# Kernel tuning notes

Hardware: AMD Instinct MI355X
Metric: run time of the kernel (lower is better)

Reference implementation:

```python
import jax, jax.numpy as jnp
import numpy as np

N = 50000
E = 600000
D = 128


def setup_inputs() -> dict:
    key = jax.random.key(0)
    ks = jax.random.split(key, 10)
    scale = 1.0 / np.sqrt(D)
    inp = {
        "x": jax.random.normal(ks[0], (N, D), dtype=jnp.float32),
        "edge_index": jax.random.randint(ks[1], (2, E), 0, N, dtype=jnp.int64),
        # layer 0: fc + res_fc (residual=True, activation=relu)
        "W1": jax.random.normal(ks[2], (D, D), dtype=jnp.float32) * scale,
        "R1": jax.random.normal(ks[3], (D, D), dtype=jnp.float32) * scale,
        # layer 1
        "W2": jax.random.normal(ks[4], (D, D), dtype=jnp.float32) * scale,
        "R2": jax.random.normal(ks[5], (D, D), dtype=jnp.float32) * scale,
        # layer 2 (last, encoding=False -> no residual/activation)
        "W3": jax.random.normal(ks[6], (D, D), dtype=jnp.float32) * scale,
        # head Linear(out_dim, out_dim) with bias
        "Wh": jax.random.normal(ks[7], (D, D), dtype=jnp.float32) * scale,
        "bh": jnp.zeros((D,), dtype=jnp.float32),
    }
    return inp


def _gcn_stack(x, row, col, norm, W1, R1, W2, R2, W3, Wh, bh):
    n = x.shape[0]

    def conv(x, W, R, act):
        h = x @ W                                   # [N, D]
        msg = h[row] * norm[:, None]                # gather + per-edge scale [E+N, D]
        agg = jax.ops.segment_sum(msg, col, num_segments=n)  # scatter-add [N, D]
        if R is not None:
            agg = agg + x @ R                       # residual
        if act:
            agg = jax.nn.relu(agg)
        return agg

    x = conv(x, W1, R1, True)
    x = conv(x, W2, R2, True)
    x = conv(x, W3, None, False)
    return x @ Wh + bh


def reference(x, edge_index, W1, R1, W2, R2, W3, Wh, bh):
    n = x.shape[0]
    # add self loops (same edge structure for every layer)
    loops = jnp.arange(n, dtype=edge_index.dtype)
    row = jnp.concatenate([edge_index[0], loops])
    col = jnp.concatenate([edge_index[1], loops])
    # symmetric degree normalization: deg computed over col (incl. self loops)
    deg = jax.ops.segment_sum(jnp.ones_like(col, dtype=x.dtype), col, num_segments=n)
    dinv = deg ** -0.5
    norm = dinv[row] * dinv[col]                    # [E+N]
    return _gcn_stack(x, row, col, norm, W1, R1, W2, R2, W3, Wh, bh)
```

## Files before the change

### kernel.cpp

```cpp
#include <hip/hip_runtime.h>
#include <hip/hip_bf16.h>


#define SCAN_CHUNK 1024

typedef _Float16 half8 __attribute__((ext_vector_type(8)));
typedef _Float16 half4 __attribute__((ext_vector_type(4)));
typedef float floatx4 __attribute__((ext_vector_type(4)));

__global__ __launch_bounds__(256) void prep0_kernel(
        int* __restrict__ cnt, int n, int nzb,
        const float* __restrict__ W1, const float* __restrict__ R1,
        const float* __restrict__ W2, const float* __restrict__ R2,
        const float* __restrict__ W3, const float* __restrict__ Wh,
        _Float16* __restrict__ Wt) {
    int b = blockIdx.x;
    int t = threadIdx.x;
    if (b < nzb) {
        int i = b * 256 + t;
        if (i < n) cnt[i] = 0;
        return;
    }
    int b2 = b - nzb;
    if (b2 < 64) {
        __shared__ float tile[32][33];
        int mat = b2 >> 4, tl = b2 & 15;
        const float* W = (mat == 0) ? W1 : (mat == 1) ? R1 : (mat == 2) ? W2 : R2;
        _Float16* T = Wt + (size_t)mat * 16384;
        int tr = (tl >> 2) * 32, tc = (tl & 3) * 32;
        int i = t >> 3, j4 = t & 7;
        float4 v = *(const float4*)&W[(tr + i) * 128 + tc + j4 * 4];
        tile[i][j4 * 4 + 0] = v.x;
        tile[i][j4 * 4 + 1] = v.y;
        tile[i][j4 * 4 + 2] = v.z;
        tile[i][j4 * 4 + 3] = v.w;
        __syncthreads();
        half4 h;
        h.x = (_Float16)tile[j4 * 4 + 0][i];
        h.y = (_Float16)tile[j4 * 4 + 1][i];
        h.z = (_Float16)tile[j4 * 4 + 2][i];
        h.w = (_Float16)tile[j4 * 4 + 3][i];
        *(half4*)&T[(tc + i) * 128 + tr + j4 * 4] = h;
    } else {
        int bb = b2 - 64;
        _Float16* Wtc = Wt + (size_t)4 * 16384;
        int c = bb * 8 + (t >> 5);
        int k0 = (t & 31) * 4;
        float acc0 = 0.f, acc1 = 0.f, acc2 = 0.f, acc3 = 0.f;
        for (int j = 0; j < 128; ++j) {
            float wh = Wh[j * 128 + c];
            acc0 = fmaf(W3[(k0 + 0) * 128 + j], wh, acc0);
            acc1 = fmaf(W3[(k0 + 1) * 128 + j], wh, acc1);
            acc2 = fmaf(W3[(k0 + 2) * 128 + j], wh, acc2);
            acc3 = fmaf(W3[(k0 + 3) * 128 + j], wh, acc3);
        }
        half4 h;
        h.x = (_Float16)acc0; h.y = (_Float16)acc1;
        h.z = (_Float16)acc2; h.w = (_Float16)acc3;
        *(half4*)&Wtc[c * 128 + k0] = h;
    }
}

__global__ void hist_kernel(const int* __restrict__ col, int* __restrict__ cnt, int E) {
    int i = blockIdx.x * blockDim.x + threadIdx.x;
    if (i < E) atomicAdd(&cnt[col[i]], 1);
}

__global__ __launch_bounds__(256) void scan_fused_kernel(
        const int* __restrict__ cnt, int* __restrict__ row_ptr,
        int* __restrict__ cursor, float* __restrict__ dinv, int n, int E) {
    __shared__ int s[256];
    int b = blockIdx.x, t = threadIdx.x;

    int tot = 0;
    int lim = b * SCAN_CHUNK;
    for (int i = t * 4; i < lim; i += 1024) {
        int4 q = *(const int4*)&cnt[i];
        tot += q.x + q.y + q.z + q.w;
    }
    s[t] = tot;
    __syncthreads();
    for (int off = 128; off > 0; off >>= 1) {
        if (t < off) s[t] += s[t + off];
        __syncthreads();
    }
    int boffb = s[0];
    __syncthreads();

    int base = b * SCAN_CHUNK + t * 4;
    int v[4];
    int sum = 0;
    for (int i = 0; i < 4; ++i) {
        v[i] = (base + i < n) ? cnt[base + i] : 0;
        sum += v[i];
    }
    s[t] = sum;
    __syncthreads();
    for (int off = 1; off < 256; off <<= 1) {
        int add = (t >= off) ? s[t - off] : 0;
        __syncthreads();
        s[t] += add;
        __syncthreads();
    }
    int prefix = boffb + ((t == 0) ? 0 : s[t - 1]);
    for (int i = 0; i < 4; ++i) {
        if (base + i < n) {
            row_ptr[base + i] = prefix;
            cursor[base + i] = prefix;
            dinv[base + i] = rsqrtf((float)(v[i] + 1));
            prefix += v[i];
        }
    }
    if (b == 0 && t == 0) row_ptr[n] = E;
}

__global__ void fill_kernel(const int* __restrict__ row, const int* __restrict__ colv,
                            int* __restrict__ cursor,
                            unsigned short* __restrict__ csr, int E) {
    int i = blockIdx.x * blockDim.x + threadIdx.x;
    if (i < E) {
        int c = colv[i];
        int p = atomicAdd(&cursor[c], 1);
        csr[p] = (unsigned short)row[i];
    }
}

template <int F32IN>
__global__ __launch_bounds__(256) void gemm_dual_kernel(
        const void* __restrict__ Xv, const _Float16* __restrict__ WtA,
        const _Float16* __restrict__ WtB, _Float16* __restrict__ outA,
        _Float16* __restrict__ outB, const float* __restrict__ dinv, int n) {
    __shared__ _Float16 Af[64 * 136];
    __shared__ _Float16 Bt[128 * 136];
    int t = threadIdx.x;
    int r0 = blockIdx.x * 64;

    if (F32IN) {
        const float* X = (const float*)Xv;
#pragma unroll
        for (int i = 0; i < 8; ++i) {
            int flat = i * 256 + t;
            int r = flat >> 5, c4 = flat & 31;
            float4 v = make_float4(0.f, 0.f, 0.f, 0.f);
            if (r0 + r < n) v = ((const float4*)X)[(size_t)(r0 + r) * 32 + c4];
            half4 h;
            h.x = (_Float16)v.x; h.y = (_Float16)v.y;
            h.z = (_Float16)v.z; h.w = (_Float16)v.w;
            *(half4*)&Af[r * 136 + c4 * 4] = h;
        }
    } else {
        const _Float16* X = (const _Float16*)Xv;
#pragma unroll
        for (int i = 0; i < 4; ++i) {
            int flat = i * 256 + t;
            int r = flat >> 4, k8 = flat & 15;
            half8 v = {0, 0, 0, 0, 0, 0, 0, 0};
            if (r0 + r < n) v = *(const half8*)&X[(size_t)(r0 + r) * 128 + k8 * 8];
            *(half8*)&Af[r * 136 + k8 * 8] = v;
        }
    }
#pragma unroll
    for (int i = 0; i < 8; ++i) {
        int flat = i * 256 + t;
        int c = flat >> 4, k8 = flat & 15;
        *(half8*)&Bt[c * 136 + k8 * 8] = *(const half8*)&WtA[c * 128 + k8 * 8];
    }
    __syncthreads();

    int lane = t & 63, w = t >> 6;
    int m = lane & 15, q = lane >> 4;
    int rowb = r0 + w * 16 + q * 4;

    float dv[4];
#pragma unroll
    for (int r = 0; r < 4; ++r) {
        int gr = rowb + r;
        dv[r] = (gr < n) ? dinv[gr] : 0.f;
    }

    half8 a[4];
#pragma unroll
    for (int s = 0; s < 4; ++s)
        a[s] = *(const half8*)&Af[(w * 16 + m) * 136 + s * 32 + q * 8];

    floatx4 acc[8];
#pragma unroll
    for (int nt = 0; nt < 8; ++nt) acc[nt] = (floatx4){0.f, 0.f, 0.f, 0.f};
#pragma unroll
    for (int s = 0; s < 4; ++s)
#pragma unroll
        for (int nt = 0; nt < 8; ++nt) {
            half8 b = *(const half8*)&Bt[(nt * 16 + m) * 136 + s * 32 + q * 8];
            acc[nt] = __builtin_amdgcn_mfma_f32_16x16x32_f16(a[s], b, acc[nt], 0, 0, 0);
        }
    __syncthreads();
#pragma unroll
    for (int i = 0; i < 8; ++i) {
        int flat = i * 256 + t;
        int c = flat >> 4, k8 = flat & 15;
        *(half8*)&Bt[c * 136 + k8 * 8] = *(const half8*)&WtB[c * 128 + k8 * 8];
    }
#pragma unroll
    for (int nt = 0; nt < 8; ++nt) {
        int col = nt * 16 + m;
#pragma unroll
        for (int r = 0; r < 4; ++r) {
            int gr = rowb + r;
            if (gr < n) outA[(size_t)gr * 128 + col] = (_Float16)(acc[nt][r] * dv[r]);
        }
    }
    __syncthreads();

#pragma unroll
    for (int nt = 0; nt < 8; ++nt) acc[nt] = (floatx4){0.f, 0.f, 0.f, 0.f};
#pragma unroll
    for (int s = 0; s < 4; ++s)
#pragma unroll
        for (int nt = 0; nt < 8; ++nt) {
            half8 b = *(const half8*)&Bt[(nt * 16 + m) * 136 + s * 32 + q * 8];
            acc[nt] = __builtin_amdgcn_mfma_f32_16x16x32_f16(a[s], b, acc[nt], 0, 0, 0);
        }
#pragma unroll
    for (int nt = 0; nt < 8; ++nt) {
        int col = nt * 16 + m;
#pragma unroll
        for (int r = 0; r < 4; ++r) {
            int gr = rowb + r;
            if (gr < n) outB[(size_t)gr * 128 + col] = (_Float16)acc[nt][r];
        }
    }
}

__global__ __launch_bounds__(256) void gemm_h_kernel(
        const _Float16* __restrict__ X, const _Float16* __restrict__ Wt,
        _Float16* __restrict__ out, const float* __restrict__ dinv, int n) {
    __shared__ _Float16 Af[64 * 136];
    __shared__ _Float16 Bt[128 * 136];
    int t = threadIdx.x;
    int r0 = blockIdx.x * 64;

#pragma unroll
    for (int i = 0; i < 4; ++i) {
        int flat = i * 256 + t;
        int r = flat >> 4, k8 = flat & 15;
        half8 v = {0, 0, 0, 0, 0, 0, 0, 0};
        if (r0 + r < n) v = *(const half8*)&X[(size_t)(r0 + r) * 128 + k8 * 8];
        *(half8*)&Af[r * 136 + k8 * 8] = v;
    }
#pragma unroll
    for (int i = 0; i < 8; ++i) {
        int flat = i * 256 + t;
        int c = flat >> 4, k8 = flat & 15;
        *(half8*)&Bt[c * 136 + k8 * 8] = *(const half8*)&Wt[c * 128 + k8 * 8];
    }
    __syncthreads();

    int lane = t & 63, w = t >> 6;
    int m = lane & 15, q = lane >> 4;
    int rowb = r0 + w * 16 + q * 4;

    float dv[4];
#pragma unroll
    for (int r = 0; r < 4; ++r) {
        int gr = rowb + r;
        dv[r] = (gr < n) ? dinv[gr] : 0.f;
    }

    floatx4 acc[8];
#pragma unroll
    for (int nt = 0; nt < 8; ++nt) acc[nt] = (floatx4){0.f, 0.f, 0.f, 0.f};

#pragma unroll
    for (int s = 0; s < 4; ++s) {
        half8 a = *(const half8*)&Af[(w * 16 + m) * 136 + s * 32 + q * 8];
#pragma unroll
        for (int nt = 0; nt < 8; ++nt) {
            half8 b = *(const half8*)&Bt[(nt * 16 + m) * 136 + s * 32 + q * 8];
            acc[nt] = __builtin_amdgcn_mfma_f32_16x16x32_f16(a, b, acc[nt], 0, 0, 0);
        }
    }

#pragma unroll
    for (int nt = 0; nt < 8; ++nt) {
        int col = nt * 16 + m;
#pragma unroll
        for (int r = 0; r < 4; ++r) {
            int gr = rowb + r;
            if (gr < n) out[(size_t)gr * 128 + col] = (_Float16)(acc[nt][r] * dv[r]);
        }
    }
}

template <int RELU, int FINAL>
__global__ void spmm_kernel(const _Float16* __restrict__ h, const _Float16* __restrict__ xr,
                            const int* __restrict__ row_ptr,
                            const unsigned short* __restrict__ csr,
                            const float* __restrict__ dinv, _Float16* __restrict__ outh,
                            float* __restrict__ outf, const float* __restrict__ bias,
                            int n) {
    int gid = blockIdx.x * blockDim.x + threadIdx.x;
    int node = gid >> 4;
    int fl = gid & 15;
    if (node >= n) return;
    const half8* hp8 = (const half8*)h;

    float acc[8];
#pragma unroll
    for (int j = 0; j < 8; ++j) acc[j] = 0.f;

    int e0 = row_ptr[node], e1 = row_ptr[node + 1];
    for (int e = e0; e < e1; e += 8) {
        int src[8];
        float nn[8];
#pragma unroll
        for (int u = 0; u < 8; ++u) {
            int idx = e + u;
            int act = idx < e1;
            src[u] = csr[act ? idx : e];
            nn[u] = act ? 1.f : 0.f;
        }
        half8 v[8];
#pragma unroll
        for (int u = 0; u < 8; ++u)
            v[u] = hp8[(size_t)src[u] * 16 + fl];
#pragma unroll
        for (int u = 0; u < 8; ++u)
#pragma unroll
            for (int j = 0; j < 8; ++j)
                acc[j] = fmaf(nn[u], (float)v[u][j], acc[j]);
    }

    float di = dinv[node];
    half8 hv = hp8[(size_t)node * 16 + fl];
#pragma unroll
    for (int j = 0; j < 8; ++j) acc[j] += (float)hv[j];
#pragma unroll
    for (int j = 0; j < 8; ++j) acc[j] *= di;

    if (!FINAL && xr) {
        half8 r = ((const half8*)xr)[(size_t)node * 16 + fl];
#pragma unroll
        for (int j = 0; j < 8; ++j) acc[j] += (float)r[j];
    }
    if (RELU) {
#pragma unroll
        for (int j = 0; j < 8; ++j) acc[j] = fmaxf(acc[j], 0.f);
    }
    if (FINAL) {
        float4 b0 = *(const float4*)&bias[fl * 8];
        float4 b1 = *(const float4*)&bias[fl * 8 + 4];
        float4 o0 = make_float4(acc[0] + b0.x, acc[1] + b0.y,
                                acc[2] + b0.z, acc[3] + b0.w);
        float4 o1 = make_float4(acc[4] + b1.x, acc[5] + b1.y,
                                acc[6] + b1.z, acc[7] + b1.w);
        ((float4*)outf)[(size_t)node * 32 + fl * 2] = o0;
        ((float4*)outf)[(size_t)node * 32 + fl * 2 + 1] = o1;
    } else {
        half8 o;
#pragma unroll
        for (int j = 0; j < 8; ++j) o[j] = (_Float16)acc[j];
        ((half8*)outh)[(size_t)node * 16 + fl] = o;
    }
}

extern "C" void kernel_launch(void* const* d_in, const int* in_sizes, int n_in,
                              void* d_out, int out_size, void* d_ws, size_t ws_size,
                              hipStream_t stream) {
    const float* x  = (const float*)d_in[0];
    const int*   ei = (const int*)d_in[1];
    const float* W1 = (const float*)d_in[2];
    const float* R1 = (const float*)d_in[3];
    const float* W2 = (const float*)d_in[4];
    const float* R2 = (const float*)d_in[5];
    const float* W3 = (const float*)d_in[6];
    const float* Wh = (const float*)d_in[7];
    const float* bh = (const float*)d_in[8];
    float* out = (float*)d_out;

    int N = in_sizes[0] / 128;
    int E = in_sizes[1] / 2;

    char* p = (char*)d_ws;
    auto alloc = [&](size_t bytes) {
        char* r = p;
        p += (bytes + 255) & ~(size_t)255;
        return r;
    };
    int*            cnt     = (int*)alloc((size_t)N * 4);
    int*            row_ptr = (int*)alloc((size_t)(N + 1) * 4);
    int*            cursor  = (int*)alloc((size_t)N * 4);
    float*          dinv    = (float*)alloc((size_t)N * 4);
    unsigned short* csr     = (unsigned short*)alloc((size_t)E * 2);
    _Float16*       Wt      = (_Float16*)alloc((size_t)5 * 16384 * 2);
    _Float16*       B0h     = (_Float16*)alloc((size_t)N * 128 * 2);
    _Float16*       B1h     = (_Float16*)alloc((size_t)N * 128 * 2);
    _Float16*       B2h     = (_Float16*)alloc((size_t)N * 128 * 2);

    const int* rowi = ei;
    const int* coli = ei + E;

    int nb = (N + SCAN_CHUNK - 1) / SCAN_CHUNK;
    int nzb = (N + 255) / 256;

    prep0_kernel<<<nzb + 80, 256, 0, stream>>>(cnt, N, nzb, W1, R1, W2, R2, W3, Wh, Wt);
    hist_kernel<<<(E + 255) / 256, 256, 0, stream>>>(coli, cnt, E);
    scan_fused_kernel<<<nb, 256, 0, stream>>>(cnt, row_ptr, cursor, dinv, N, E);
    fill_kernel<<<(E + 255) / 256, 256, 0, stream>>>(rowi, coli, cursor, csr, E);

    int gb = (N + 63) / 64;
    int sb = ((size_t)N * 16 + 255) / 256;
    _Float16* Wt1 = Wt;
    _Float16* Rt1 = Wt + 16384;
    _Float16* Wt2 = Wt + 2 * 16384;
    _Float16* Rt2 = Wt + 3 * 16384;
    _Float16* Wtc = Wt + 4 * 16384;

    gemm_dual_kernel<1><<<gb, 256, 0, stream>>>(x, Wt1, Rt1, B0h, B1h, dinv, N);
    spmm_kernel<1, 0><<<sb, 256, 0, stream>>>(B0h, B1h, row_ptr, csr, dinv,
                                              B1h, nullptr, nullptr, N);
    gemm_dual_kernel<0><<<gb, 256, 0, stream>>>(B1h, Wt2, Rt2, B0h, B2h, dinv, N);
    spmm_kernel<1, 0><<<sb, 256, 0, stream>>>(B0h, B2h, row_ptr, csr, dinv,
                                              B2h, nullptr, nullptr, N);
    gemm_h_kernel<<<gb, 256, 0, stream>>>(B2h, Wtc, B0h, dinv, N);
    spmm_kernel<0, 1><<<sb, 256, 0, stream>>>(B0h, nullptr, row_ptr, csr, dinv,
                                              nullptr, out, bh, N);
}
```

Measured before the change: 298.5 us.

## Pad CSR segments to multiples of eight with dummy zero row for vector index loads

Each node's CSR segment is padded to a multiple of 8 entries. Padding slots are pre-filled with index N, which points at an extra all-zero row appended to the h buffer. This lets the SpMM load 8 indices with one vector load and drop the per-edge bounds check and mask multiply. In exchange it gathers extra zero rows for the padding slots, enlarges the workspace, and adds fill work in the prep kernel. It also limits node ids to 16 bits.

```diff
diff --git a/kernel.cpp b/kernel.cpp
--- a/kernel.cpp
+++ b/kernel.cpp
@@ -7,13 +7,15 @@
 typedef _Float16 half8 __attribute__((ext_vector_type(8)));
 typedef _Float16 half4 __attribute__((ext_vector_type(4)));
 typedef float floatx4 __attribute__((ext_vector_type(4)));
+typedef unsigned short ushort8 __attribute__((ext_vector_type(8)));
 
 __global__ __launch_bounds__(256) void prep0_kernel(
         int* __restrict__ cnt, int n, int nzb,
         const float* __restrict__ W1, const float* __restrict__ R1,
         const float* __restrict__ W2, const float* __restrict__ R2,
         const float* __restrict__ W3, const float* __restrict__ Wh,
-        _Float16* __restrict__ Wt) {
+        _Float16* __restrict__ Wt, _Float16* __restrict__ B0h,
+        unsigned* __restrict__ csru, unsigned pat) {
     int b = blockIdx.x;
     int t = threadIdx.x;
     if (b < nzb) {
@@ -41,7 +43,7 @@
         h.z = (_Float16)tile[j4 * 4 + 2][i];
         h.w = (_Float16)tile[j4 * 4 + 3][i];
         *(half4*)&T[(tc + i) * 128 + tr + j4 * 4] = h;
-    } else {
+    } else if (b2 < 80) {
         int bb = b2 - 64;
         _Float16* Wtc = Wt + (size_t)4 * 16384;
         int c = bb * 8 + (t >> 5);
@@ -58,6 +60,15 @@
         h.x = (_Float16)acc0; h.y = (_Float16)acc1;
         h.z = (_Float16)acc2; h.w = (_Float16)acc3;
         *(half4*)&Wtc[c * 128 + k0] = h;
+    } else if (b2 == 80) {
+        if (t < 16) {
+            half8 z = {0, 0, 0, 0, 0, 0, 0, 0};
+            ((half8*)B0h)[(size_t)n * 16 + t] = z;
+        }
+    } else {
+        size_t o = ((size_t)(b2 - 81) * 256 + t) * 4;
+        uint4 p4 = make_uint4(pat, pat, pat, pat);
+        *(uint4*)&csru[o] = p4;
     }
 }
 
@@ -68,7 +79,7 @@
 
 __global__ __launch_bounds__(256) void scan_fused_kernel(
         const int* __restrict__ cnt, int* __restrict__ row_ptr,
-        int* __restrict__ cursor, float* __restrict__ dinv, int n, int E) {
+        int* __restrict__ cursor, float* __restrict__ dinv, int n, int nb) {
     __shared__ int s[256];
     int b = blockIdx.x, t = threadIdx.x;
 
@@ -76,7 +87,8 @@
     int lim = b * SCAN_CHUNK;
     for (int i = t * 4; i < lim; i += 1024) {
         int4 q = *(const int4*)&cnt[i];
-        tot += q.x + q.y + q.z + q.w;
+        tot += ((q.x + 7) & ~7) + ((q.y + 7) & ~7)
+             + ((q.z + 7) & ~7) + ((q.w + 7) & ~7);
     }
     s[t] = tot;
     __syncthreads();
@@ -88,11 +100,12 @@
     __syncthreads();
 
     int base = b * SCAN_CHUNK + t * 4;
-    int v[4];
+    int v[4], sl[4];
     int sum = 0;
     for (int i = 0; i < 4; ++i) {
         v[i] = (base + i < n) ? cnt[base + i] : 0;
-        sum += v[i];
+        sl[i] = (v[i] + 7) & ~7;
+        sum += sl[i];
     }
     s[t] = sum;
     __syncthreads();
@@ -108,10 +121,10 @@
             row_ptr[base + i] = prefix;
             cursor[base + i] = prefix;
             dinv[base + i] = rsqrtf((float)(v[i] + 1));
-            prefix += v[i];
-        }
-    }
-    if (b == 0 && t == 0) row_ptr[n] = E;
+            prefix += sl[i];
+        }
+    }
+    if (b == nb - 1 && t == 255) row_ptr[n] = prefix;
 }
 
 __global__ void fill_kernel(const int* __restrict__ row, const int* __restrict__ colv,
@@ -308,26 +321,21 @@
 #pragma unroll
     for (int j = 0; j < 8; ++j) acc[j] = 0.f;
 
+    float one;
+    asm("v_mov_b32 %0, 1.0" : "=v"(one));
+
     int e0 = row_ptr[node], e1 = row_ptr[node + 1];
     for (int e = e0; e < e1; e += 8) {
-        int src[8];
-        float nn[8];
-#pragma unroll
-        for (int u = 0; u < 8; ++u) {
-            int idx = e + u;
-            int act = idx < e1;
-            src[u] = csr[act ? idx : e];
-            nn[u] = act ? 1.f : 0.f;
-        }
+        ushort8 d8 = *(const ushort8*)&csr[e];
         half8 v[8];
 #pragma unroll
         for (int u = 0; u < 8; ++u)
-            v[u] = hp8[(size_t)src[u] * 16 + fl];
+            v[u] = hp8[(size_t)d8[u] * 16 + fl];
 #pragma unroll
         for (int u = 0; u < 8; ++u)
 #pragma unroll
             for (int j = 0; j < 8; ++j)
-                acc[j] = fmaf(nn[u], (float)v[u][j], acc[j]);
+                acc[j] = fmaf(one, (float)v[u][j], acc[j]);
     }
 
     float di = dinv[node];
@@ -380,6 +388,11 @@
     int N = in_sizes[0] / 128;
     int E = in_sizes[1] / 2;
 
+    size_t csr_entries = (size_t)E + 7 * (size_t)N + 8;
+    size_t csr_uints = (csr_entries + 1) / 2;
+    int pfb = (int)((csr_uints + 1023) / 1024);
+    csr_uints = (size_t)pfb * 1024;
+
     char* p = (char*)d_ws;
     auto alloc = [&](size_t bytes) {
         char* r = p;
@@ -390,9 +403,10 @@
     int*            row_ptr = (int*)alloc((size_t)(N + 1) * 4);
     int*            cursor  = (int*)alloc((size_t)N * 4);
     float*          dinv    = (float*)alloc((size_t)N * 4);
-    unsigned short* csr     = (unsigned short*)alloc((size_t)E * 2);
+    unsigned*       csru    = (unsigned*)alloc(csr_uints * 4);
+    unsigned short* csr     = (unsigned short*)csru;
     _Float16*       Wt      = (_Float16*)alloc((size_t)5 * 16384 * 2);
-    _Float16*       B0h     = (_Float16*)alloc((size_t)N * 128 * 2);
+    _Float16*       B0h     = (_Float16*)alloc((size_t)(N + 1) * 128 * 2);
     _Float16*       B1h     = (_Float16*)alloc((size_t)N * 128 * 2);
     _Float16*       B2h     = (_Float16*)alloc((size_t)N * 128 * 2);
 
@@ -401,10 +415,12 @@
 
     int nb = (N + SCAN_CHUNK - 1) / SCAN_CHUNK;
     int nzb = (N + 255) / 256;
-
-    prep0_kernel<<<nzb + 80, 256, 0, stream>>>(cnt, N, nzb, W1, R1, W2, R2, W3, Wh, Wt);
+    unsigned pat = (unsigned)N * 0x10001u;
+
+    prep0_kernel<<<nzb + 81 + pfb, 256, 0, stream>>>(
+        cnt, N, nzb, W1, R1, W2, R2, W3, Wh, Wt, B0h, csru, pat);
     hist_kernel<<<(E + 255) / 256, 256, 0, stream>>>(coli, cnt, E);
-    scan_fused_kernel<<<nb, 256, 0, stream>>>(cnt, row_ptr, cursor, dinv, N, E);
+    scan_fused_kernel<<<nb, 256, 0, stream>>>(cnt, row_ptr, cursor, dinv, N, nb);
     fill_kernel<<<(E + 255) / 256, 256, 0, stream>>>(rowi, coli, cursor, csr, E);
 
     int gb = (N + 63) / 64;
```

Result: no change. 303.6 us (+1.7%).

## Fuse histogram into first GEMM, pack edge weights into CSR, degree-bucket node order

Applied to the files above, without the earlier changes.

The first dense GEMM no longer depends on dinv. It is merged with the degree histogram into one launch, removing a kernel and letting the atomics overlap with matrix work. Per-edge source normalisation is stored as an fp16 weight packed beside the source index in a 32-bit CSR entry, so the GEMMs drop their dinv scaling and the self-loop term is scaled by dinv at aggregation instead. Nodes are also permuted into degree buckets so SpMM threads in a wave have similar loop trip counts. The cost is a wider CSR array, an extra indirection through perm, and fp16 rounding of the normalisation weights.

```diff
diff --git a/kernel.cpp b/kernel.cpp
--- a/kernel.cpp
+++ b/kernel.cpp
@@ -7,13 +7,18 @@
 typedef _Float16 half8 __attribute__((ext_vector_type(8)));
 typedef _Float16 half4 __attribute__((ext_vector_type(4)));
 typedef float floatx4 __attribute__((ext_vector_type(4)));
+
+__device__ __forceinline__ int bucket_of(int deg) {
+    int c = (deg + 7) >> 3;
+    return c < 7 ? c : 7;
+}
 
 __global__ __launch_bounds__(256) void prep0_kernel(
         int* __restrict__ cnt, int n, int nzb,
         const float* __restrict__ W1, const float* __restrict__ R1,
         const float* __restrict__ W2, const float* __restrict__ R2,
         const float* __restrict__ W3, const float* __restrict__ Wh,
-        _Float16* __restrict__ Wt) {
+        _Float16* __restrict__ Wt, int* __restrict__ bstat) {
     int b = blockIdx.x;
     int t = threadIdx.x;
     if (b < nzb) {
@@ -41,7 +46,7 @@
         h.z = (_Float16)tile[j4 * 4 + 2][i];
         h.w = (_Float16)tile[j4 * 4 + 3][i];
         *(half4*)&T[(tc + i) * 128 + tr + j4 * 4] = h;
-    } else {
+    } else if (b2 < 80) {
         int bb = b2 - 64;
         _Float16* Wtc = Wt + (size_t)4 * 16384;
         int c = bb * 8 + (t >> 5);
@@ -58,19 +63,111 @@
         h.x = (_Float16)acc0; h.y = (_Float16)acc1;
         h.z = (_Float16)acc2; h.w = (_Float16)acc3;
         *(half4*)&Wtc[c * 128 + k0] = h;
-    }
-}
-
-__global__ void hist_kernel(const int* __restrict__ col, int* __restrict__ cnt, int E) {
-    int i = blockIdx.x * blockDim.x + threadIdx.x;
-    if (i < E) atomicAdd(&cnt[col[i]], 1);
+    } else {
+        if (t < 16) bstat[t] = 0;
+    }
+}
+
+__global__ __launch_bounds__(256) void gemm1_hist_kernel(
+        const float* __restrict__ X, const _Float16* __restrict__ WtA,
+        const _Float16* __restrict__ WtB, _Float16* __restrict__ outA,
+        _Float16* __restrict__ outB, int n, int gb,
+        const int* __restrict__ col, int* __restrict__ cnt, int E) {
+    __shared__ _Float16 Af[64 * 136];
+    __shared__ _Float16 Bt[128 * 136];
+    int t = threadIdx.x;
+    int b = blockIdx.x;
+    if (b >= gb) {
+        int i = (b - gb) * 256 + t;
+        if (i < E) atomicAdd(&cnt[col[i]], 1);
+        return;
+    }
+    int r0 = b * 64;
+
+#pragma unroll
+    for (int i = 0; i < 8; ++i) {
+        int flat = i * 256 + t;
+        int r = flat >> 5, c4 = flat & 31;
+        float4 v = make_float4(0.f, 0.f, 0.f, 0.f);
+        if (r0 + r < n) v = ((const float4*)X)[(size_t)(r0 + r) * 32 + c4];
+        half4 h;
+        h.x = (_Float16)v.x; h.y = (_Float16)v.y;
+        h.z = (_Float16)v.z; h.w = (_Float16)v.w;
+        *(half4*)&Af[r * 136 + c4 * 4] = h;
+    }
+#pragma unroll
+    for (int i = 0; i < 8; ++i) {
+        int flat = i * 256 + t;
+        int c = flat >> 4, k8 = flat & 15;
+        *(half8*)&Bt[c * 136 + k8 * 8] = *(const half8*)&WtA[c * 128 + k8 * 8];
+    }
+    __syncthreads();
+
+    int lane = t & 63, w = t >> 6;
+    int m = lane & 15, q = lane >> 4;
+    int rowb = r0 + w * 16 + q * 4;
+
+    half8 a[4];
+#pragma unroll
+    for (int s = 0; s < 4; ++s)
+        a[s] = *(const half8*)&Af[(w * 16 + m) * 136 + s * 32 + q * 8];
+
+    floatx4 acc[8];
+#pragma unroll
+    for (int nt = 0; nt < 8; ++nt) acc[nt] = (floatx4){0.f, 0.f, 0.f, 0.f};
+#pragma unroll
+    for (int s = 0; s < 4; ++s)
+#pragma unroll
+        for (int nt = 0; nt < 8; ++nt) {
+            half8 bb = *(const half8*)&Bt[(nt * 16 + m) * 136 + s * 32 + q * 8];
+            acc[nt] = __builtin_amdgcn_mfma_f32_16x16x32_f16(a[s], bb, acc[nt], 0, 0, 0);
+        }
+    __syncthreads();
+#pragma unroll
+    for (int i = 0; i < 8; ++i) {
+        int flat = i * 256 + t;
+        int c = flat >> 4, k8 = flat & 15;
+        *(half8*)&Bt[c * 136 + k8 * 8] = *(const half8*)&WtB[c * 128 + k8 * 8];
+    }
+#pragma unroll
+    for (int nt = 0; nt < 8; ++nt) {
+        int col0 = nt * 16 + m;
+#pragma unroll
+        for (int r = 0; r < 4; ++r) {
+            int gr = rowb + r;
+            if (gr < n) outA[(size_t)gr * 128 + col0] = (_Float16)acc[nt][r];
+        }
+    }
+    __syncthreads();
+
+#pragma unroll
+    for (int nt = 0; nt < 8; ++nt) acc[nt] = (floatx4){0.f, 0.f, 0.f, 0.f};
+#pragma unroll
+    for (int s = 0; s < 4; ++s)
+#pragma unroll
+        for (int nt = 0; nt < 8; ++nt) {
+            half8 bb = *(const half8*)&Bt[(nt * 16 + m) * 136 + s * 32 + q * 8];
+            acc[nt] = __builtin_amdgcn_mfma_f32_16x16x32_f16(a[s], bb, acc[nt], 0, 0, 0);
+        }
+#pragma unroll
+    for (int nt = 0; nt < 8; ++nt) {
+        int col0 = nt * 16 + m;
+#pragma unroll
+        for (int r = 0; r < 4; ++r) {
+            int gr = rowb + r;
+            if (gr < n) outB[(size_t)gr * 128 + col0] = (_Float16)acc[nt][r];
+        }
+    }
 }
 
 __global__ __launch_bounds__(256) void scan_fused_kernel(
         const int* __restrict__ cnt, int* __restrict__ row_ptr,
-        int* __restrict__ cursor, float* __restrict__ dinv, int n, int E) {
+        int* __restrict__ cursor, float* __restrict__ dinv,
+        int* __restrict__ bcnt, int n, int E) {
     __shared__ int s[256];
+    __shared__ int bh[8];
     int b = blockIdx.x, t = threadIdx.x;
+    if (t < 8) bh[t] = 0;
 
     int tot = 0;
     int lim = b * SCAN_CHUNK;
@@ -93,6 +190,7 @@
     for (int i = 0; i < 4; ++i) {
         v[i] = (base + i < n) ? cnt[base + i] : 0;
         sum += v[i];
+        if (base + i < n) atomicAdd(&bh[bucket_of(v[i])], 1);
     }
     s[t] = sum;
     __syncthreads();
@@ -112,58 +210,72 @@
         }
     }
     if (b == 0 && t == 0) row_ptr[n] = E;
-}
-
-__global__ void fill_kernel(const int* __restrict__ row, const int* __restrict__ colv,
-                            int* __restrict__ cursor,
-                            unsigned short* __restrict__ csr, int E) {
-    int i = blockIdx.x * blockDim.x + threadIdx.x;
-    if (i < E) {
-        int c = colv[i];
-        int p = atomicAdd(&cursor[c], 1);
-        csr[p] = (unsigned short)row[i];
-    }
-}
-
-template <int F32IN>
-__global__ __launch_bounds__(256) void gemm_dual_kernel(
-        const void* __restrict__ Xv, const _Float16* __restrict__ WtA,
-        const _Float16* __restrict__ WtB, _Float16* __restrict__ outA,
-        _Float16* __restrict__ outB, const float* __restrict__ dinv, int n) {
+    if (t < 8 && bh[t]) atomicAdd(&bcnt[t], bh[t]);
+}
+
+__global__ __launch_bounds__(256) void fill_place_kernel(
+        const int* __restrict__ row, const int* __restrict__ colv,
+        const float* __restrict__ dinv, int* __restrict__ cursor,
+        unsigned* __restrict__ csr, int E, int eb,
+        const int* __restrict__ cnt, const int* __restrict__ bcnt,
+        int* __restrict__ bcur, int* __restrict__ perm, int n) {
+    int b = blockIdx.x, t = threadIdx.x;
+    if (b < eb) {
+        int i = b * 256 + t;
+        if (i < E) {
+            int r = row[i], c = colv[i];
+            int p = atomicAdd(&cursor[c], 1);
+            _Float16 w = (_Float16)dinv[r];
+            csr[p] = (unsigned)r |
+                     ((unsigned)__builtin_bit_cast(unsigned short, w) << 16);
+        }
+        return;
+    }
+    __shared__ int bh[8];
+    __shared__ int bbase[8];
+    int i = (b - eb) * 256 + t;
+    if (t < 8) bh[t] = 0;
+    __syncthreads();
+    int bk = 0, rank = 0;
+    if (i < n) {
+        bk = bucket_of(cnt[i]);
+        rank = atomicAdd(&bh[bk], 1);
+    }
+    __syncthreads();
+    if (t < 8) {
+        int cb = bh[t];
+        int base = 0;
+#pragma unroll
+        for (int j = 0; j < 8; ++j)
+            if (j < t) base += bcnt[j];
+        int off = cb ? atomicAdd(&bcur[t], cb) : 0;
+        bbase[t] = base + off;
+    }
+    __syncthreads();
+    if (i < n) perm[bbase[bk] + rank] = i;
+}
+
+__global__ __launch_bounds__(256) void gemm_h_kernel(
+        const _Float16* __restrict__ X, const _Float16* __restrict__ Wt,
+        _Float16* __restrict__ out, int n) {
     __shared__ _Float16 Af[64 * 136];
     __shared__ _Float16 Bt[128 * 136];
     int t = threadIdx.x;
     int r0 = blockIdx.x * 64;
 
-    if (F32IN) {
-        const float* X = (const float*)Xv;
-#pragma unroll
-        for (int i = 0; i < 8; ++i) {
-            int flat = i * 256 + t;
-            int r = flat >> 5, c4 = flat & 31;
-            float4 v = make_float4(0.f, 0.f, 0.f, 0.f);
-            if (r0 + r < n) v = ((const float4*)X)[(size_t)(r0 + r) * 32 + c4];
-            half4 h;
-            h.x = (_Float16)v.x; h.y = (_Float16)v.y;
-            h.z = (_Float16)v.z; h.w = (_Float16)v.w;
-            *(half4*)&Af[r * 136 + c4 * 4] = h;
-        }
-    } else {
-        const _Float16* X = (const _Float16*)Xv;
-#pragma unroll
-        for (int i = 0; i < 4; ++i) {
-            int flat = i * 256 + t;
-            int r = flat >> 4, k8 = flat & 15;
-            half8 v = {0, 0, 0, 0, 0, 0, 0, 0};
-            if (r0 + r < n) v = *(const half8*)&X[(size_t)(r0 + r) * 128 + k8 * 8];
-            *(half8*)&Af[r * 136 + k8 * 8] = v;
-        }
+#pragma unroll
+    for (int i = 0; i < 4; ++i) {
+        int flat = i * 256 + t;
+        int r = flat >> 4, k8 = flat & 15;
+        half8 v = {0, 0, 0, 0, 0, 0, 0, 0};
+        if (r0 + r < n) v = *(const half8*)&X[(size_t)(r0 + r) * 128 + k8 * 8];
+        *(half8*)&Af[r * 136 + k8 * 8] = v;
     }
 #pragma unroll
     for (int i = 0; i < 8; ++i) {
         int flat = i * 256 + t;
         int c = flat >> 4, k8 = flat & 15;
-        *(half8*)&Bt[c * 136 + k8 * 8] = *(const half8*)&WtA[c * 128 + k8 * 8];
+        *(half8*)&Bt[c * 136 + k8 * 8] = *(const half8*)&Wt[c * 128 + k8 * 8];
     }
     __syncthreads();
 
@@ -171,69 +283,35 @@
     int m = lane & 15, q = lane >> 4;
     int rowb = r0 + w * 16 + q * 4;
 
-    float dv[4];
-#pragma unroll
-    for (int r = 0; r < 4; ++r) {
-        int gr = rowb + r;
-        dv[r] = (gr < n) ? dinv[gr] : 0.f;
-    }
-
-    half8 a[4];
-#pragma unroll
-    for (int s = 0; s < 4; ++s)
-        a[s] = *(const half8*)&Af[(w * 16 + m) * 136 + s * 32 + q * 8];
-
     floatx4 acc[8];
 #pragma unroll
     for (int nt = 0; nt < 8; ++nt) acc[nt] = (floatx4){0.f, 0.f, 0.f, 0.f};
-#pragma unroll
-    for (int s = 0; s < 4; ++s)
+
+#pragma unroll
+    for (int s = 0; s < 4; ++s) {
+        half8 a = *(const half8*)&Af[(w * 16 + m) * 136 + s * 32 + q * 8];
 #pragma unroll
         for (int nt = 0; nt < 8; ++nt) {
-            half8 b = *(const half8*)&Bt[(nt * 16 + m) * 136 + s * 32 + q * 8];
-            acc[nt] = __builtin_amdgcn_mfma_f32_16x16x32_f16(a[s], b, acc[nt], 0, 0, 0);
-        }
-    __syncthreads();
-#pragma unroll
-    for (int i = 0; i < 8; ++i) {
-        int flat = i * 256 + t;
-        int c = flat >> 4, k8 = flat & 15;
-        *(half8*)&Bt[c * 136 + k8 * 8] = *(const half8*)&WtB[c * 128 + k8 * 8];
-    }
+            half8 bb = *(const half8*)&Bt[(nt * 16 + m) * 136 + s * 32 + q * 8];
+            acc[nt] = __builtin_amdgcn_mfma_f32_16x16x32_f16(a, bb, acc[nt], 0, 0, 0);
+        }
+    }
+
 #pragma unroll
     for (int nt = 0; nt < 8; ++nt) {
         int col = nt * 16 + m;
 #pragma unroll
         for (int r = 0; r < 4; ++r) {
             int gr = rowb + r;
-            if (gr < n) outA[(size_t)gr * 128 + col] = (_Float16)(acc[nt][r] * dv[r]);
-        }
-    }
-    __syncthreads();
-
-#pragma unroll
-    for (int nt = 0; nt < 8; ++nt) acc[nt] = (floatx4){0.f, 0.f, 0.f, 0.f};
-#pragma unroll
-    for (int s = 0; s < 4; ++s)
-#pragma unroll
-        for (int nt = 0; nt < 8; ++nt) {
-            half8 b = *(const half8*)&Bt[(nt * 16 + m) * 136 + s * 32 + q * 8];
-            acc[nt] = __builtin_amdgcn_mfma_f32_16x16x32_f16(a[s], b, acc[nt], 0, 0, 0);
-        }
-#pragma unroll
-    for (int nt = 0; nt < 8; ++nt) {
-        int col = nt * 16 + m;
-#pragma unroll
-        for (int r = 0; r < 4; ++r) {
-            int gr = rowb + r;
-            if (gr < n) outB[(size_t)gr * 128 + col] = (_Float16)acc[nt][r];
-        }
-    }
-}
-
-__global__ __launch_bounds__(256) void gemm_h_kernel(
-        const _Float16* __restrict__ X, const _Float16* __restrict__ Wt,
-        _Float16* __restrict__ out, const float* __restrict__ dinv, int n) {
+            if (gr < n) out[(size_t)gr * 128 + col] = (_Float16)acc[nt][r];
+        }
+    }
+}
+
+__global__ __launch_bounds__(256) void gemm_dual_h_kernel(
+        const _Float16* __restrict__ X, const _Float16* __restrict__ WtA,
+        const _Float16* __restrict__ WtB, _Float16* __restrict__ outA,
+        _Float16* __restrict__ outB, int n) {
     __shared__ _Float16 Af[64 * 136];
     __shared__ _Float16 Bt[128 * 136];
     int t = threadIdx.x;
@@ -251,7 +329,7 @@
     for (int i = 0; i < 8; ++i) {
         int flat = i * 256 + t;
         int c = flat >> 4, k8 = flat & 15;
-        *(half8*)&Bt[c * 136 + k8 * 8] = *(const half8*)&Wt[c * 128 + k8 * 8];
+        *(half8*)&Bt[c * 136 + k8 * 8] = *(const half8*)&WtA[c * 128 + k8 * 8];
     }
     __syncthreads();
 
@@ -259,34 +337,55 @@
     int m = lane & 15, q = lane >> 4;
     int rowb = r0 + w * 16 + q * 4;
 
-    float dv[4];
-#pragma unroll
-    for (int r = 0; r < 4; ++r) {
-        int gr = rowb + r;
-        dv[r] = (gr < n) ? dinv[gr] : 0.f;
-    }
+    half8 a[4];
+#pragma unroll
+    for (int s = 0; s < 4; ++s)
+        a[s] = *(const half8*)&Af[(w * 16 + m) * 136 + s * 32 + q * 8];
 
     floatx4 acc[8];
 #pragma unroll
     for (int nt = 0; nt < 8; ++nt) acc[nt] = (floatx4){0.f, 0.f, 0.f, 0.f};
-
-#pragma unroll
-    for (int s = 0; s < 4; ++s) {
-        half8 a = *(const half8*)&Af[(w * 16 + m) * 136 + s * 32 + q * 8];
+#pragma unroll
+    for (int s = 0; s < 4; ++s)
 #pragma unroll
         for (int nt = 0; nt < 8; ++nt) {
-            half8 b = *(const half8*)&Bt[(nt * 16 + m) * 136 + s * 32 + q * 8];
-            acc[nt] = __builtin_amdgcn_mfma_f32_16x16x32_f16(a, b, acc[nt], 0, 0, 0);
-        }
-    }
-
+            half8 bb = *(const half8*)&Bt[(nt * 16 + m) * 136 + s * 32 + q * 8];
+            acc[nt] = __builtin_amdgcn_mfma_f32_16x16x32_f16(a[s], bb, acc[nt], 0, 0, 0);
+        }
+    __syncthreads();
+#pragma unroll
+    for (int i = 0; i < 8; ++i) {
+        int flat = i * 256 + t;
+        int c = flat >> 4, k8 = flat & 15;
+        *(half8*)&Bt[c * 136 + k8 * 8] = *(const half8*)&WtB[c * 128 + k8 * 8];
+    }
 #pragma unroll
     for (int nt = 0; nt < 8; ++nt) {
         int col = nt * 16 + m;
 #pragma unroll
         for (int r = 0; r < 4; ++r) {
             int gr = rowb + r;
-            if (gr < n) out[(size_t)gr * 128 + col] = (_Float16)(acc[nt][r] * dv[r]);
+            if (gr < n) outA[(size_t)gr * 128 + col] = (_Float16)acc[nt][r];
+        }
+    }
+    __syncthreads();
+
+#pragma unroll
+    for (int nt = 0; nt < 8; ++nt) acc[nt] = (floatx4){0.f, 0.f, 0.f, 0.f};
+#pragma unroll
+    for (int s = 0; s < 4; ++s)
+#pragma unroll
+        for (int nt = 0; nt < 8; ++nt) {
+            half8 bb = *(const half8*)&Bt[(nt * 16 + m) * 136 + s * 32 + q * 8];
+            acc[nt] = __builtin_amdgcn_mfma_f32_16x16x32_f16(a[s], bb, acc[nt], 0, 0, 0);
+        }
+#pragma unroll
+    for (int nt = 0; nt < 8; ++nt) {
+        int col = nt * 16 + m;
+#pragma unroll
+        for (int r = 0; r < 4; ++r) {
+            int gr = rowb + r;
+            if (gr < n) outB[(size_t)gr * 128 + col] = (_Float16)acc[nt][r];
         }
     }
 }
@@ -294,14 +393,17 @@
 template <int RELU, int FINAL>
 __global__ void spmm_kernel(const _Float16* __restrict__ h, const _Float16* __restrict__ xr,
                             const int* __restrict__ row_ptr,
-                            const unsigned short* __restrict__ csr,
-                            const float* __restrict__ dinv, _Float16* __restrict__ outh,
+                            const unsigned* __restrict__ csr,
+                            const float* __restrict__ dinv,
+                            const int* __restrict__ perm,
+                            _Float16* __restrict__ outh,
                             float* __restrict__ outf, const float* __restrict__ bias,
                             int n) {
     int gid = blockIdx.x * blockDim.x + threadIdx.x;
-    int node = gid >> 4;
+    int sub = gid >> 4;
     int fl = gid & 15;
-    if (node >= n) return;
+    if (sub >= n) return;
+    int node = perm[sub];
     const half8* hp8 = (const half8*)h;
 
     float acc[8];
@@ -310,19 +412,20 @@
 
     int e0 = row_ptr[node], e1 = row_ptr[node + 1];
     for (int e = e0; e < e1; e += 8) {
-        int src[8];
+        unsigned d[8];
         float nn[8];
 #pragma unroll
         for (int u = 0; u < 8; ++u) {
             int idx = e + u;
             int act = idx < e1;
-            src[u] = csr[act ? idx : e];
-            nn[u] = act ? 1.f : 0.f;
+            d[u] = csr[act ? idx : e0];
+            nn[u] = act ? (float)__builtin_bit_cast(_Float16, (unsigned short)(d[u] >> 16))
+                        : 0.f;
         }
         half8 v[8];
 #pragma unroll
         for (int u = 0; u < 8; ++u)
-            v[u] = hp8[(size_t)src[u] * 16 + fl];
+            v[u] = hp8[(size_t)(d[u] & 0xffffu) * 16 + fl];
 #pragma unroll
         for (int u = 0; u < 8; ++u)
 #pragma unroll
@@ -333,7 +436,7 @@
     float di = dinv[node];
     half8 hv = hp8[(size_t)node * 16 + fl];
 #pragma unroll
-    for (int j = 0; j < 8; ++j) acc[j] += (float)hv[j];
+    for (int j = 0; j < 8; ++j) acc[j] = fmaf(di, (float)hv[j], acc[j]);
 #pragma unroll
     for (int j = 0; j < 8; ++j) acc[j] *= di;
 
@@ -386,42 +489,51 @@
         p += (bytes + 255) & ~(size_t)255;
         return r;
     };
-    int*            cnt     = (int*)alloc((size_t)N * 4);
-    int*            row_ptr = (int*)alloc((size_t)(N + 1) * 4);
-    int*            cursor  = (int*)alloc((size_t)N * 4);
-    float*          dinv    = (float*)alloc((size_t)N * 4);
-    unsigned short* csr     = (unsigned short*)alloc((size_t)E * 2);
-    _Float16*       Wt      = (_Float16*)alloc((size_t)5 * 16384 * 2);
-    _Float16*       B0h     = (_Float16*)alloc((size_t)N * 128 * 2);
-    _Float16*       B1h     = (_Float16*)alloc((size_t)N * 128 * 2);
-    _Float16*       B2h     = (_Float16*)alloc((size_t)N * 128 * 2);
+    int*      cnt     = (int*)alloc((size_t)N * 4);
+    int*      row_ptr = (int*)alloc((size_t)(N + 1) * 4);
+    int*      cursor  = (int*)alloc((size_t)N * 4);
+    float*    dinv    = (float*)alloc((size_t)N * 4);
+    int*      perm    = (int*)alloc((size_t)N * 4);
+    int*      bstat   = (int*)alloc((size_t)16 * 4);
+    unsigned* csr     = (unsigned*)alloc((size_t)E * 4);
+    _Float16* Wt      = (_Float16*)alloc((size_t)5 * 16384 * 2);
+    _Float16* B0h     = (_Float16*)alloc((size_t)N * 128 * 2);
+    _Float16* B1h     = (_Float16*)alloc((size_t)N * 128 * 2);
+    _Float16* B2h     = (_Float16*)alloc((size_t)N * 128 * 2);
+
+    int* bcnt = bstat;
+    int* bcur = bstat + 8;
 
     const int* rowi = ei;
     const int* coli = ei + E;
 
-    int nb = (N + SCAN_CHUNK - 1) / SCAN_CHUNK;
+    int nb  = (N + SCAN_CHUNK - 1) / SCAN_CHUNK;
     int nzb = (N + 255) / 256;
-
-    prep0_kernel<<<nzb + 80, 256, 0, stream>>>(cnt, N, nzb, W1, R1, W2, R2, W3, Wh, Wt);
-    hist_kernel<<<(E + 255) / 256, 256, 0, stream>>>(coli, cnt, E);
-    scan_fused_kernel<<<nb, 256, 0, stream>>>(cnt, row_ptr, cursor, dinv, N, E);
-    fill_kernel<<<(E + 255) / 256, 256, 0, stream>>>(rowi, coli, cursor, csr, E);
-
-    int gb = (N + 63) / 64;
-    int sb = ((size_t)N * 16 + 255) / 256;
+    int eb  = (E + 255) / 256;
+    int pb  = (N + 255) / 256;
+    int gb  = (N + 63) / 64;
+    int sb  = ((size_t)N * 16 + 255) / 256;
+
     _Float16* Wt1 = Wt;
     _Float16* Rt1 = Wt + 16384;
     _Float16* Wt2 = Wt + 2 * 16384;
     _Float16* Rt2 = Wt + 3 * 16384;
     _Float16* Wtc = Wt + 4 * 16384;
 
-    gemm_dual_kernel<1><<<gb, 256, 0, stream>>>(x, Wt1, Rt1, B0h, B1h, dinv, N);
-    spmm_kernel<1, 0><<<sb, 256, 0, stream>>>(B0h, B1h, row_ptr, csr, dinv,
+    prep0_kernel<<<nzb + 81, 256, 0, stream>>>(cnt, N, nzb, W1, R1, W2, R2, W3, Wh,
+                                               Wt, bstat);
+    gemm1_hist_kernel<<<gb + eb, 256, 0, stream>>>(x, Wt1, Rt1, B0h, B1h, N, gb,
+                                                   coli, cnt, E);
+    scan_fused_kernel<<<nb, 256, 0, stream>>>(cnt, row_ptr, cursor, dinv, bcnt, N, E);
+    fill_place_kernel<<<eb + pb, 256, 0, stream>>>(rowi, coli, dinv, cursor, csr,
+                                                   E, eb, cnt, bcnt, bcur, perm, N);
+
+    spmm_kernel<1, 0><<<sb, 256, 0, stream>>>(B0h, B1h, row_ptr, csr, dinv, perm,
                                               B1h, nullptr, nullptr, N);
-    gemm_dual_kernel<0><<<gb, 256, 0, stream>>>(B1h, Wt2, Rt2, B0h, B2h, dinv, N);
-    spmm_kernel<1, 0><<<sb, 256, 0, stream>>>(B0h, B2h, row_ptr, csr, dinv,
+    gemm_dual_h_kernel<<<gb, 256, 0, stream>>>(B1h, Wt2, Rt2, B0h, B2h, N);
+    spmm_kernel<1, 0><<<sb, 256, 0, stream>>>(B0h, B2h, row_ptr, csr, dinv, perm,
                                               B2h, nullptr, nullptr, N);
-    gemm_h_kernel<<<gb, 256, 0, stream>>>(B2h, Wtc, B0h, dinv, N);
-    spmm_kernel<0, 1><<<sb, 256, 0, stream>>>(B0h, nullptr, row_ptr, csr, dinv,
+    gemm_h_kernel<<<gb, 256, 0, stream>>>(B2h, Wtc, B0h, N);
+    spmm_kernel<0, 1><<<sb, 256, 0, stream>>>(B0h, nullptr, row_ptr, csr, dinv, perm,
                                               nullptr, out, bh, N);
 }
```

New measurement: 297.6 us. About the same (-0.3%).
